# Kernel optimization log

Measured on AMD Instinct MI355X. Metric: run time of the kernel, lower is better.

## Reference

```python
import jax, jax.numpy as jnp
import numpy as np

B, T, C, H = 2, 2048, 1024, 16
D = C // H  # head_dim = 64


def setup_inputs() -> dict:
    key = jax.random.key(0)
    ks = jax.random.split(key, 5)
    s = 1.0 / np.sqrt(C)
    return {
        "x": jax.random.normal(ks[0], (B, T, C), jnp.float32),
        "Wq": jax.random.normal(ks[1], (C, C), jnp.float32) * s,
        "bq": jnp.zeros((C,), jnp.float32),
        "Wk": jax.random.normal(ks[2], (C, C), jnp.float32) * s,
        "bk": jnp.zeros((C,), jnp.float32),
        "Wv": jax.random.normal(ks[3], (C, C), jnp.float32) * s,
        "bv": jnp.zeros((C,), jnp.float32),
        "Wo": jax.random.normal(ks[4], (C, C), jnp.float32) * s,
        "bo": jnp.zeros((C,), jnp.float32),
    }


def reference(x, Wq, bq, Wk, bk, Wv, bv, Wo, bo):
    Bx, Tx, Cx = x.shape
    # torch Linear: y = x @ W.T + b
    q = (x @ Wq.T + bq).reshape(Bx, Tx, H, D).transpose(0, 2, 1, 3)  # [B,H,T,D]
    k = (x @ Wk.T + bk).reshape(Bx, Tx, H, D).transpose(0, 2, 1, 3)
    v = (x @ Wv.T + bv).reshape(Bx, Tx, H, D).transpose(0, 2, 1, 3)
    att = jnp.einsum("bhqd,bhkd->bhqk", q, k) / np.sqrt(D).astype(np.float32)
    mask = jnp.tril(jnp.ones((Tx, Tx), bool))  # causal mask [T,T]
    att = jnp.where(mask, att, -jnp.inf)
    att = jax.nn.softmax(att, axis=-1)
    out = jnp.einsum("bhqk,bhkd->bhqd", att, v)
    out = out.transpose(0, 2, 1, 3).reshape(Bx, Tx, Cx)
    return out @ Wo.T + bo
```

## Files before the change

### kernel.cpp

```cpp
#include <hip/hip_runtime.h>
#include <hip/hip_bf16.h>

#define B_ 2
#define T_ 2048
#define C_ 1024
#define H_ 16
#define D_ 64

typedef unsigned short u16;
typedef __bf16 bf16x8 __attribute__((ext_vector_type(8)));
typedef float floatx4 __attribute__((ext_vector_type(4)));

__device__ __forceinline__ float bf2f(u16 u) {
  union { unsigned int i; float f; } x; x.i = ((unsigned int)u) << 16; return x.f;
}
__device__ __forceinline__ u16 f2bf(float f) {
  union { float f; unsigned int i; } x; x.f = f;
  unsigned int r = x.i + 0x7fffu + ((x.i >> 16) & 1u);
  return (u16)(r >> 16);
}

__device__ __forceinline__ unsigned cvtpk(float lo, float hi) {
  unsigned r;
  asm("v_cvt_pk_bf16_f32 %0, %1, %2" : "=v"(r) : "v"(lo), "v"(hi));
  return r;
}

__device__ __forceinline__ void gld16(void* lds, const void* g) {
  __builtin_amdgcn_global_load_lds(
      (const __attribute__((address_space(1))) unsigned int*)g,
      (__attribute__((address_space(3))) unsigned int*)lds, 16, 0, 0);
}

#define NXF4 1048576
#define NWF4 262144

__global__ __launch_bounds__(256) void cvt_all(
    const float* __restrict__ x,  const float* __restrict__ Wq,
    const float* __restrict__ Wk, const float* __restrict__ Wv,
    const float* __restrict__ Wo, u16* __restrict__ dst_base)
{
  const int i = blockIdx.x * 256 + threadIdx.x;
  const float* src; size_t off;
  if (i < NXF4)               { src = x;  off = i; }
  else if (i < NXF4 + NWF4)   { src = Wq; off = i - NXF4; }
  else if (i < NXF4 + 2*NWF4) { src = Wk; off = i - (NXF4 + NWF4); }
  else if (i < NXF4 + 3*NWF4) { src = Wv; off = i - (NXF4 + 2*NWF4); }
  else                        { src = Wo; off = i - (NXF4 + 3*NWF4); }
  float4 f = ((const float4*)src)[off];
  ushort4 o;
  o.x = f2bf(f.x); o.y = f2bf(f.y); o.z = f2bf(f.z); o.w = f2bf(f.w);
  ((ushort4*)dst_base)[i] = o;
}

#define QSCALE 0.1803368801111f

#define MFMA16(MH, NH, BREG)                                                  \
  do {                                                                        \
    __builtin_amdgcn_s_setprio(1);                                            \
    _Pragma("unroll")                                                         \
    for (int f = 0; f < 4; ++f) {                                             \
      _Pragma("unroll")                                                       \
      for (int g = 0; g < 2; ++g) {                                           \
        acc[(MH)*4 + f][(NH)*2 + g] = __builtin_amdgcn_mfma_f32_16x16x32_bf16(\
            a[f][0], BREG[g][0], acc[(MH)*4 + f][(NH)*2 + g], 0, 0, 0);       \
        acc[(MH)*4 + f][(NH)*2 + g] = __builtin_amdgcn_mfma_f32_16x16x32_bf16(\
            a[f][1], BREG[g][1], acc[(MH)*4 + f][(NH)*2 + g], 0, 0, 0);       \
      }                                                                       \
    }                                                                         \
    __builtin_amdgcn_s_setprio(0);                                            \
  } while (0)

#define PBAR()                                                \
  do {                                                        \
    asm volatile("" ::: "memory");                            \
    __builtin_amdgcn_s_barrier();                             \
    asm volatile("s_waitcnt lgkmcnt(0)" ::: "memory");        \
  } while (0)

#define EBAR()                                                \
  do {                                                        \
    asm volatile("" ::: "memory");                            \
    __builtin_amdgcn_s_barrier();                             \
    asm volatile("" ::: "memory");                            \
  } while (0)

__global__ __launch_bounds__(512, 2) void gemm_qkv8(
    const u16* __restrict__ X, const u16* __restrict__ Wb,
    const float* __restrict__ b0, const float* __restrict__ b1,
    const float* __restrict__ b2,
    u16* __restrict__ Yq, u16* __restrict__ Yk, u16* __restrict__ Yv)
{
  __shared__ __align__(16) u16 L[65536];

  const int tid  = threadIdx.x;
  const int lane = tid & 63;
  const int m16  = lane & 15;
  const int q4   = lane >> 4;
  const int wv   = tid >> 6;
  const int wm   = wv >> 2;
  const int wn   = wv & 3;

  const int bid = blockIdx.x;
  const int xcd = bid & 7;
  const int idx = bid >> 3;
  const int bx  = (xcd & 3) * 4 + (idx & 3);
  const int by  = (xcd >> 2) * 6 + (idx >> 2);

  const u16* Abase  = X  + (size_t)bx * 256 * C_;
  const u16* Bbase  = Wb + (size_t)by * 256 * C_;
  const u16* A1base = Abase + (size_t)128 * C_;
  const u16* B1base = Bbase + (size_t)128 * C_;

  const int s0 = tid,       r0 = s0 >> 3;
  const int s1 = tid + 512, r1 = s1 >> 3;
  const int k0a = ((s0 & 7) ^ (r0 & 7)) * 8;
  const int k1a = ((s1 & 7) ^ (r1 & 7)) * 8;

#define STAGE(dsthalf, srcrows, kofs)                                         \
  do {                                                                        \
    gld16(&(dsthalf)[s0 * 8], (srcrows) + (size_t)r0 * C_ + (kofs) + k0a);    \
    gld16(&(dsthalf)[s1 * 8], (srcrows) + (size_t)r1 * C_ + (kofs) + k1a);    \
  } while (0)

  u16* buf0 = L;
  u16* buf1 = L + 32768;

  STAGE(buf0 + 16384, Bbase, 0);
  STAGE(buf0,         Abase, 0);
  STAGE(buf0 + 24576, B1base, 0);
  STAGE(buf0 + 8192,  A1base, 0);
  STAGE(buf1 + 16384, Bbase, 64);
  STAGE(buf1,         Abase, 64);
  asm volatile("s_waitcnt vmcnt(4)" ::: "memory");
  __builtin_amdgcn_s_barrier();
  asm volatile("" ::: "memory");

  floatx4 acc[8][4] = {};

  const int a0off = m16 * 64 + ((q4      ^ (lane & 7)) * 8);
  const int a1off = m16 * 64 + (((q4 + 4) ^ (lane & 7)) * 8);
  const int bro   = (wn & 1) * 4096;

  for (int i = 0; i < 16; ++i) {
    u16* buf  = (i & 1) ? buf1 : buf0;
    u16* bufn = (i & 1) ? buf0 : buf1;
    const u16* Ah = buf + wm * 8192;
    const u16* Bh = buf + 16384 + (wn >> 1) * 8192;
    const bool p1 = (i + 1) < 16;
    const bool p2 = (i + 2) < 16;
    const int  k1 = (i + 1) * 64;
    const int  k2 = (i + 2) * 64;

    bf16x8 a[4][2], bA[2][2], bB[2][2];

#pragma unroll
    for (int f = 0; f < 4; ++f) {
      a[f][0] = *(const bf16x8*)&Ah[f * 1024 + a0off];
      a[f][1] = *(const bf16x8*)&Ah[f * 1024 + a1off];
    }
#pragma unroll
    for (int g = 0; g < 2; ++g) {
      bA[g][0] = *(const bf16x8*)&Bh[bro + g * 1024 + a0off];
      bA[g][1] = *(const bf16x8*)&Bh[bro + g * 1024 + a1off];
    }
    if (p1) STAGE(bufn + 24576, B1base, k1);
    PBAR();
    MFMA16(0, 0, bA);
    EBAR();

#pragma unroll
    for (int g = 0; g < 2; ++g) {
      bB[g][0] = *(const bf16x8*)&Bh[bro + 2048 + g * 1024 + a0off];
      bB[g][1] = *(const bf16x8*)&Bh[bro + 2048 + g * 1024 + a1off];
    }
    if (p1) STAGE(bufn + 8192, A1base, k1);
    PBAR();
    MFMA16(0, 1, bB);
    EBAR();

#pragma unroll
    for (int f = 0; f < 4; ++f) {
      a[f][0] = *(const bf16x8*)&Ah[4096 + f * 1024 + a0off];
      a[f][1] = *(const bf16x8*)&Ah[4096 + f * 1024 + a1off];
    }
    if (p2) STAGE(buf + 16384, Bbase, k2);
    PBAR();
    MFMA16(1, 1, bB);
    EBAR();

    if (p2) STAGE(buf, Abase, k2);
    PBAR();
    MFMA16(1, 0, bA);
    asm volatile("" ::: "memory");
    if (p2) asm volatile("s_waitcnt vmcnt(4)" ::: "memory");
    else    asm volatile("s_waitcnt vmcnt(0)" ::: "memory");
    __builtin_amdgcn_s_barrier();
    asm volatile("" ::: "memory");
  }

  const int z    = by >> 2;
  const int nloc = (by & 3) * 256 + wn * 64;
  const float* bias = (z == 0) ? b0 : (z == 1) ? b1 : b2;
  const int mbase = bx * 256 + wm * 128 + q4 * 4;

  if (z == 2) {
#pragma unroll
    for (int nf = 0; nf < 4; ++nf) {
      const int nz = nloc + nf * 16 + m16;
      const float bv = bias[nz];
      const int h = nz >> 6, d = nz & (D_ - 1);
#pragma unroll
      for (int mf = 0; mf < 8; ++mf) {
        const int m  = mbase + mf * 16;
        const int bb = m >> 11, t = m & (T_ - 1);
        ushort4 pk;
        pk.x = f2bf(acc[mf][nf][0] + bv);
        pk.y = f2bf(acc[mf][nf][1] + bv);
        pk.z = f2bf(acc[mf][nf][2] + bv);
        pk.w = f2bf(acc[mf][nf][3] + bv);
        *(ushort4*)&Yv[(((size_t)bb * H_ + h) * D_ + d) * T_ + t] = pk;
      }
    }
  } else {
    u16* Y = z ? Yk : Yq;
    const float sc = z ? 1.0f : QSCALE;
#pragma unroll
    for (int nf = 0; nf < 4; ++nf) {
      const int nz = nloc + nf * 16 + m16;
      const float bv = bias[nz];
      const int h = nz >> 6, d = nz & (D_ - 1);
#pragma unroll
      for (int mf = 0; mf < 8; ++mf) {
        const int m  = mbase + mf * 16;
        const int bb = m >> 11, tq = m & (T_ - 1);
#pragma unroll
        for (int r = 0; r < 4; ++r) {
          Y[(((size_t)bb * H_ + h) * T_ + (tq + r)) * D_ + d] =
              f2bf((acc[mf][nf][r] + bv) * sc);
        }
      }
    }
  }
}

__global__ __launch_bounds__(256) void gemm_out(
    const u16* __restrict__ X, const u16* __restrict__ W,
    const float* __restrict__ bias, float* __restrict__ Yf)
{
  const int K = C_, N = C_;
  __shared__ __align__(16) u16 As[128 * 32];
  __shared__ __align__(16) u16 Bs[64 * 32];

  const int tid  = threadIdx.x;
  const int wv   = tid >> 6;
  const int lane = tid & 63;
  const int mcol = lane & 15;
  const int quad = lane >> 4;
  const int wr = wv >> 1, wc = wv & 1;
  const int m0 = blockIdx.x * 128;
  const int n0 = blockIdx.y * 64;

  const int srow = tid >> 2;
  const int scol = (tid & 3) * 8;
  const u16* xp0 = X + (size_t)(m0 + srow) * K + scol;
  const u16* xp1 = xp0 + (size_t)64 * K;
  const u16* wp  = W + (size_t)(n0 + srow) * K + scol;

  floatx4 acc[4][2] = {};

  for (int k0 = 0; k0 < K; k0 += 32) {
    gld16(&As[tid * 8],        xp0 + k0);
    gld16(&As[2048 + tid * 8], xp1 + k0);
    gld16(&Bs[tid * 8],        wp + k0);
    __syncthreads();

    bf16x8 a[4], b[2];
#pragma unroll
    for (int rf = 0; rf < 4; ++rf)
      a[rf] = *(const bf16x8*)&As[(wr * 64 + rf * 16 + mcol) * 32 + quad * 8];
#pragma unroll
    for (int cf = 0; cf < 2; ++cf)
      b[cf] = *(const bf16x8*)&Bs[(wc * 32 + cf * 16 + mcol) * 32 + quad * 8];
#pragma unroll
    for (int rf = 0; rf < 4; ++rf)
#pragma unroll
      for (int cf = 0; cf < 2; ++cf)
        acc[rf][cf] = __builtin_amdgcn_mfma_f32_16x16x32_bf16(
            a[rf], b[cf], acc[rf][cf], 0, 0, 0);
    __syncthreads();
  }

#pragma unroll
  for (int cf = 0; cf < 2; ++cf) {
    const int n = n0 + wc * 32 + cf * 16 + mcol;
    const float bv = bias[n];
#pragma unroll
    for (int rf = 0; rf < 4; ++rf) {
#pragma unroll
      for (int r = 0; r < 4; ++r) {
        const int m = m0 + wr * 64 + rf * 16 + quad * 4 + r;
        Yf[(size_t)m * N + n] = acc[rf][cf][r] + bv;
      }
    }
  }
}

#define KSB 4096
#define VTB 5120

__global__ __launch_bounds__(256, 4) void attn_flash(
    const u16* __restrict__ Q, const u16* __restrict__ K,
    const u16* __restrict__ Vg, u16* __restrict__ O)
{
  __shared__ __align__(16) u16 Ks[2 * KSB];
  __shared__ __align__(16) u16 Vt[2 * VTB];

  const int tid  = threadIdx.x;
  const int wv   = tid >> 6;
  const int lane = tid & 63;
  const int mcol = lane & 15;
  const int quad = lane >> 4;

  const int bx = blockIdx.x;
  const int bh = bx & 31;
  const int g  = bx >> 5;
  const int ga = g & 7, gb = g >> 3;
  const int iq = (gb == 0) ? 31 - ga : (gb == 1) ? 16 + ga
               : (gb == 2) ? 15 - ga : ga;
  const size_t base  = (size_t)bh * T_ * D_;
  const size_t vbase = (size_t)bh * D_ * T_;
  const int b = bh >> 4, h = bh & (H_ - 1);

  for (int idx = tid; idx < 16 * 64; idx += 256) {
    const u16 val = (idx < 64) ? (u16)0x3F80 : (u16)0;
    Vt[64 * 64 + idx]       = val;
    Vt[VTB + 64 * 64 + idx] = val;
  }

  const int srow = lane >> 3;
  const int sg   = (lane & 7) ^ srow;
  const int c0 = wv * 2, c1 = wv * 2 + 1;
  const int sl0 = (quad ^ (mcol & 7)) * 8;

  const size_t koff0 = base + (size_t)(c0 * 8 + srow) * D_ + sg * 8;
  const size_t koff1 = base + (size_t)(c1 * 8 + srow) * D_ + sg * 8;
  const size_t voff0 = vbase + (size_t)(c0 * 8 + srow) * T_ + sg * 8;
  const size_t voff1 = vbase + (size_t)(c1 * 8 + srow) * T_ + sg * 8;

  const u16* qg = Q + base + (size_t)(iq * 64 + wv * 16 + mcol) * D_ + quad * 8;
  const bf16x8 qf0 = *(const bf16x8*)qg;
  const bf16x8 qf1 = *(const bf16x8*)(qg + 32);

  floatx4 oacc[5] = {};

  __syncthreads();
  gld16(&Ks[c0 * 512 + lane * 8], K  + koff0);
  gld16(&Ks[c1 * 512 + lane * 8], K  + koff1);
  gld16(&Vt[c0 * 512 + lane * 8], Vg + voff0);
  gld16(&Vt[c1 * 512 + lane * 8], Vg + voff1);

  for (int j = 0; j <= iq; ++j) {
    const int cur = j & 1;
    __syncthreads();

    if (j < iq) {
      const int nb = cur ^ 1;
      const size_t kj = (size_t)(j + 1) * 64 * D_;
      const int    vj = (j + 1) * 64;
      gld16(&Ks[nb * KSB + c0 * 512 + lane * 8], K  + koff0 + kj);
      gld16(&Ks[nb * KSB + c1 * 512 + lane * 8], K  + koff1 + kj);
      gld16(&Vt[nb * VTB + c0 * 512 + lane * 8], Vg + voff0 + vj);
      gld16(&Vt[nb * VTB + c1 * 512 + lane * 8], Vg + voff1 + vj);
    }

    const u16* ksb = &Ks[cur * KSB];
    const u16* vtb = &Vt[cur * VTB];

    floatx4 sacc[4] = {};
#pragma unroll
    for (int nt = 0; nt < 4; ++nt) {
      const u16* kr = &ksb[(nt * 16 + mcol) * 64];
      bf16x8 kb0 = *(const bf16x8*)&kr[sl0];
      bf16x8 kb1 = *(const bf16x8*)&kr[sl0 ^ 32];
      sacc[nt] = __builtin_amdgcn_mfma_f32_16x16x32_bf16(kb0, qf0, sacc[nt], 0, 0, 0);
      sacc[nt] = __builtin_amdgcn_mfma_f32_16x16x32_bf16(kb1, qf1, sacc[nt], 0, 0, 0);
    }

    if (j == iq) {
      const int ql = wv * 16 + mcol;
#pragma unroll
      for (int nt = 0; nt < 4; ++nt) {
#pragma unroll
        for (int r = 0; r < 4; ++r)
          if (nt * 16 + quad * 4 + r > ql) sacc[nt][r] = -1e30f;
      }
    }

    unsigned w0[2], w1[2], w2[2], w3[2];
#pragma unroll
    for (int i = 0; i < 2; ++i) {
      w0[i] = cvtpk(exp2f(sacc[0][2*i]), exp2f(sacc[0][2*i+1]));
      w1[i] = cvtpk(exp2f(sacc[1][2*i]), exp2f(sacc[1][2*i+1]));
      w2[i] = cvtpk(exp2f(sacc[2][2*i]), exp2f(sacc[2][2*i+1]));
      w3[i] = cvtpk(exp2f(sacc[3][2*i]), exp2f(sacc[3][2*i+1]));
    }

    union { unsigned u[4]; bf16x8 v; } pa0u, pa1u;
#pragma unroll
    for (int i = 0; i < 2; ++i) {
      unsigned x = w0[i], y = w1[i];
      asm("v_permlane32_swap_b32 %0, %1" : "+v"(x), "+v"(y));
      asm("v_permlane16_swap_b32 %0, %1" : "+v"(x), "+v"(y));
      pa0u.u[i] = x; pa0u.u[i + 2] = y;
      unsigned x2 = w2[i], y2 = w3[i];
      asm("v_permlane32_swap_b32 %0, %1" : "+v"(x2), "+v"(y2));
      asm("v_permlane16_swap_b32 %0, %1" : "+v"(x2), "+v"(y2));
      pa1u.u[i] = x2; pa1u.u[i + 2] = y2;
    }
    const bf16x8 pa0 = pa0u.v;
    const bf16x8 pa1 = pa1u.v;

#pragma unroll
    for (int dt = 0; dt < 5; ++dt) {
      const u16* vr = &vtb[(dt * 16 + mcol) * 64];
      bf16x8 vb0 = *(const bf16x8*)&vr[sl0];
      bf16x8 vb1 = *(const bf16x8*)&vr[sl0 ^ 32];
      oacc[dt] = __builtin_amdgcn_mfma_f32_16x16x32_bf16(pa0, vb0, oacc[dt], 0, 0, 0);
      oacc[dt] = __builtin_amdgcn_mfma_f32_16x16x32_bf16(pa1, vb1, oacc[dt], 0, 0, 0);
    }
  }

  float invl[4];
#pragma unroll
  for (int r = 0; r < 4; ++r)
    invl[r] = 1.f / __shfl(oacc[4][r], lane & 48);
#pragma unroll
  for (int dt = 0; dt < 4; ++dt) {
    const int c = h * D_ + dt * 16 + mcol;
#pragma unroll
    for (int r = 0; r < 4; ++r) {
      const int t = iq * 64 + wv * 16 + quad * 4 + r;
      O[((size_t)b * T_ + t) * C_ + c] = f2bf(oacc[dt][r] * invl[r]);
    }
  }
}

extern "C" void kernel_launch(void* const* d_in, const int* in_sizes, int n_in,
                              void* d_out, int out_size, void* d_ws, size_t ws_size,
                              hipStream_t stream) {
  const float* x  = (const float*)d_in[0];
  const float* Wq = (const float*)d_in[1];
  const float* bq = (const float*)d_in[2];
  const float* Wk = (const float*)d_in[3];
  const float* bk = (const float*)d_in[4];
  const float* Wv = (const float*)d_in[5];
  const float* bv = (const float*)d_in[6];
  const float* Wo = (const float*)d_in[7];
  const float* bo = (const float*)d_in[8];
  float* out = (float*)d_out;

  const size_t NX = (size_t)B_ * T_ * C_;
  const size_t NW = (size_t)C_ * C_;

  u16* xb  = (u16*)d_ws;
  u16* wqb = xb  + NX;
  u16* wkb = wqb + NW;
  u16* wvb = wkb + NW;
  u16* wob = wvb + NW;
  u16* q   = wob + NW;
  u16* k   = q   + NX;
  u16* v   = k   + NX;
  u16* ctx = v   + NX;

  cvt_all<<<dim3((NXF4 + 4 * NWF4) / 256), 256, 0, stream>>>(x, Wq, Wk, Wv, Wo, xb);

  gemm_qkv8<<<dim3(192), 512, 0, stream>>>(xb, wqb, bq, bk, bv, q, k, v);

  attn_flash<<<dim3(1024), 256, 0, stream>>>(q, k, v, ctx);

  gemm_out<<<dim3(32, 16), 256, 0, stream>>>(ctx, wob, bo, out);
}
```

Before: 183.4 us.

## Double attention query tile per block to reuse K/V tiles across two row groups

Each attention block now handles 128 query rows instead of 64: each wave holds two 16-row Q fragments and runs twice the MFMAs per K/V tile loaded to LDS, so K/V global and LDS traffic per query is halved. The grid shrinks to 512 blocks, the launch-bounds occupancy hint drops to 2 blocks per CU, and the block-to-query-tile ordering is simplified. MFMA sections are wrapped in s_setprio to favour matrix issue. The risks are fewer blocks, which may leave CUs underused or load-imbalanced, and higher register pressure from doubled accumulators.

```diff
diff --git a/kernel.cpp b/kernel.cpp
--- a/kernel.cpp
+++ b/kernel.cpp
@@ -309,7 +309,7 @@
 #define KSB 4096
 #define VTB 5120
 
-__global__ __launch_bounds__(256, 4) void attn_flash(
+__global__ __launch_bounds__(256, 2) void attn_flash(
     const u16* __restrict__ Q, const u16* __restrict__ K,
     const u16* __restrict__ Vg, u16* __restrict__ O)
 {
@@ -325,9 +325,7 @@
   const int bx = blockIdx.x;
   const int bh = bx & 31;
   const int g  = bx >> 5;
-  const int ga = g & 7, gb = g >> 3;
-  const int iq = (gb == 0) ? 31 - ga : (gb == 1) ? 16 + ga
-               : (gb == 2) ? 15 - ga : ga;
+  const int iq = (g < 8) ? 15 - g : g - 8;
   const size_t base  = (size_t)bh * T_ * D_;
   const size_t vbase = (size_t)bh * D_ * T_;
   const int b = bh >> 4, h = bh & (H_ - 1);
@@ -348,11 +346,15 @@
   const size_t voff0 = vbase + (size_t)(c0 * 8 + srow) * T_ + sg * 8;
   const size_t voff1 = vbase + (size_t)(c1 * 8 + srow) * T_ + sg * 8;
 
-  const u16* qg = Q + base + (size_t)(iq * 64 + wv * 16 + mcol) * D_ + quad * 8;
-  const bf16x8 qf0 = *(const bf16x8*)qg;
-  const bf16x8 qf1 = *(const bf16x8*)(qg + 32);
-
-  floatx4 oacc[5] = {};
+  const u16* qg = Q + base + (size_t)(iq * 128 + wv * 32 + mcol) * D_ + quad * 8;
+  const bf16x8 qf[2][2] = {
+    { *(const bf16x8*)qg,               *(const bf16x8*)(qg + 32) },
+    { *(const bf16x8*)(qg + 16 * D_),   *(const bf16x8*)(qg + 16 * D_ + 32) }
+  };
+
+  floatx4 oacc[2][5] = {};
+
+  const int nj = 2 * iq + 1;
 
   __syncthreads();
   gld16(&Ks[c0 * 512 + lane * 8], K  + koff0);
@@ -360,11 +362,11 @@
   gld16(&Vt[c0 * 512 + lane * 8], Vg + voff0);
   gld16(&Vt[c1 * 512 + lane * 8], Vg + voff1);
 
-  for (int j = 0; j <= iq; ++j) {
+  for (int j = 0; j <= nj; ++j) {
     const int cur = j & 1;
     __syncthreads();
 
-    if (j < iq) {
+    if (j < nj) {
       const int nb = cur ^ 1;
       const size_t kj = (size_t)(j + 1) * 64 * D_;
       const int    vj = (j + 1) * 64;
@@ -377,71 +379,85 @@
     const u16* ksb = &Ks[cur * KSB];
     const u16* vtb = &Vt[cur * VTB];
 
-    floatx4 sacc[4] = {};
+    floatx4 sacc[2][4] = {};
+    __builtin_amdgcn_s_setprio(1);
 #pragma unroll
     for (int nt = 0; nt < 4; ++nt) {
       const u16* kr = &ksb[(nt * 16 + mcol) * 64];
       bf16x8 kb0 = *(const bf16x8*)&kr[sl0];
       bf16x8 kb1 = *(const bf16x8*)&kr[sl0 ^ 32];
-      sacc[nt] = __builtin_amdgcn_mfma_f32_16x16x32_bf16(kb0, qf0, sacc[nt], 0, 0, 0);
-      sacc[nt] = __builtin_amdgcn_mfma_f32_16x16x32_bf16(kb1, qf1, sacc[nt], 0, 0, 0);
-    }
-
-    if (j == iq) {
-      const int ql = wv * 16 + mcol;
-#pragma unroll
-      for (int nt = 0; nt < 4; ++nt) {
-#pragma unroll
-        for (int r = 0; r < 4; ++r)
-          if (nt * 16 + quad * 4 + r > ql) sacc[nt][r] = -1e30f;
-      }
-    }
-
-    unsigned w0[2], w1[2], w2[2], w3[2];
-#pragma unroll
-    for (int i = 0; i < 2; ++i) {
-      w0[i] = cvtpk(exp2f(sacc[0][2*i]), exp2f(sacc[0][2*i+1]));
-      w1[i] = cvtpk(exp2f(sacc[1][2*i]), exp2f(sacc[1][2*i+1]));
-      w2[i] = cvtpk(exp2f(sacc[2][2*i]), exp2f(sacc[2][2*i+1]));
-      w3[i] = cvtpk(exp2f(sacc[3][2*i]), exp2f(sacc[3][2*i+1]));
-    }
-
-    union { unsigned u[4]; bf16x8 v; } pa0u, pa1u;
-#pragma unroll
-    for (int i = 0; i < 2; ++i) {
-      unsigned x = w0[i], y = w1[i];
-      asm("v_permlane32_swap_b32 %0, %1" : "+v"(x), "+v"(y));
-      asm("v_permlane16_swap_b32 %0, %1" : "+v"(x), "+v"(y));
-      pa0u.u[i] = x; pa0u.u[i + 2] = y;
-      unsigned x2 = w2[i], y2 = w3[i];
-      asm("v_permlane32_swap_b32 %0, %1" : "+v"(x2), "+v"(y2));
-      asm("v_permlane16_swap_b32 %0, %1" : "+v"(x2), "+v"(y2));
-      pa1u.u[i] = x2; pa1u.u[i + 2] = y2;
-    }
-    const bf16x8 pa0 = pa0u.v;
-    const bf16x8 pa1 = pa1u.v;
-
+      sacc[0][nt] = __builtin_amdgcn_mfma_f32_16x16x32_bf16(kb0, qf[0][0], sacc[0][nt], 0, 0, 0);
+      sacc[0][nt] = __builtin_amdgcn_mfma_f32_16x16x32_bf16(kb1, qf[0][1], sacc[0][nt], 0, 0, 0);
+      sacc[1][nt] = __builtin_amdgcn_mfma_f32_16x16x32_bf16(kb0, qf[1][0], sacc[1][nt], 0, 0, 0);
+      sacc[1][nt] = __builtin_amdgcn_mfma_f32_16x16x32_bf16(kb1, qf[1][1], sacc[1][nt], 0, 0, 0);
+    }
+    __builtin_amdgcn_s_setprio(0);
+
+    const int dj = j - 2 * iq;
+    if (dj >= 0) {
+#pragma unroll
+      for (int hf = 0; hf < 2; ++hf) {
+        const int klim = wv * 32 + hf * 16 + mcol - dj * 64;
+#pragma unroll
+        for (int nt = 0; nt < 4; ++nt)
+#pragma unroll
+          for (int r = 0; r < 4; ++r)
+            if (nt * 16 + quad * 4 + r > klim) sacc[hf][nt][r] = -1e30f;
+      }
+    }
+
+    bf16x8 pa[2][2];
+#pragma unroll
+    for (int hf = 0; hf < 2; ++hf) {
+      unsigned w[4][2];
+#pragma unroll
+      for (int nt = 0; nt < 4; ++nt)
+#pragma unroll
+        for (int i = 0; i < 2; ++i)
+          w[nt][i] = cvtpk(exp2f(sacc[hf][nt][2*i]), exp2f(sacc[hf][nt][2*i+1]));
+      union { unsigned u[4]; bf16x8 v; } p0, p1;
+#pragma unroll
+      for (int i = 0; i < 2; ++i) {
+        unsigned x = w[0][i], y = w[1][i];
+        asm("v_permlane32_swap_b32 %0, %1" : "+v"(x), "+v"(y));
+        asm("v_permlane16_swap_b32 %0, %1" : "+v"(x), "+v"(y));
+        p0.u[i] = x; p0.u[i + 2] = y;
+        unsigned x2 = w[2][i], y2 = w[3][i];
+        asm("v_permlane32_swap_b32 %0, %1" : "+v"(x2), "+v"(y2));
+        asm("v_permlane16_swap_b32 %0, %1" : "+v"(x2), "+v"(y2));
+        p1.u[i] = x2; p1.u[i + 2] = y2;
+      }
+      pa[hf][0] = p0.v; pa[hf][1] = p1.v;
+    }
+
+    __builtin_amdgcn_s_setprio(1);
 #pragma unroll
     for (int dt = 0; dt < 5; ++dt) {
       const u16* vr = &vtb[(dt * 16 + mcol) * 64];
       bf16x8 vb0 = *(const bf16x8*)&vr[sl0];
       bf16x8 vb1 = *(const bf16x8*)&vr[sl0 ^ 32];
-      oacc[dt] = __builtin_amdgcn_mfma_f32_16x16x32_bf16(pa0, vb0, oacc[dt], 0, 0, 0);
-      oacc[dt] = __builtin_amdgcn_mfma_f32_16x16x32_bf16(pa1, vb1, oacc[dt], 0, 0, 0);
-    }
-  }
-
-  float invl[4];
-#pragma unroll
-  for (int r = 0; r < 4; ++r)
-    invl[r] = 1.f / __shfl(oacc[4][r], lane & 48);
-#pragma unroll
-  for (int dt = 0; dt < 4; ++dt) {
-    const int c = h * D_ + dt * 16 + mcol;
-#pragma unroll
-    for (int r = 0; r < 4; ++r) {
-      const int t = iq * 64 + wv * 16 + quad * 4 + r;
-      O[((size_t)b * T_ + t) * C_ + c] = f2bf(oacc[dt][r] * invl[r]);
+      oacc[0][dt] = __builtin_amdgcn_mfma_f32_16x16x32_bf16(pa[0][0], vb0, oacc[0][dt], 0, 0, 0);
+      oacc[0][dt] = __builtin_amdgcn_mfma_f32_16x16x32_bf16(pa[0][1], vb1, oacc[0][dt], 0, 0, 0);
+      oacc[1][dt] = __builtin_amdgcn_mfma_f32_16x16x32_bf16(pa[1][0], vb0, oacc[1][dt], 0, 0, 0);
+      oacc[1][dt] = __builtin_amdgcn_mfma_f32_16x16x32_bf16(pa[1][1], vb1, oacc[1][dt], 0, 0, 0);
+    }
+    __builtin_amdgcn_s_setprio(0);
+  }
+
+#pragma unroll
+  for (int hf = 0; hf < 2; ++hf) {
+    float invl[4];
+#pragma unroll
+    for (int r = 0; r < 4; ++r)
+      invl[r] = 1.f / __shfl(oacc[hf][4][r], lane & 48);
+#pragma unroll
+    for (int dt = 0; dt < 4; ++dt) {
+      const int c = h * D_ + dt * 16 + mcol;
+#pragma unroll
+      for (int r = 0; r < 4; ++r) {
+        const int t = iq * 128 + wv * 32 + hf * 16 + quad * 4 + r;
+        O[((size_t)b * T_ + t) * C_ + c] = f2bf(oacc[hf][dt][r] * invl[r]);
+      }
     }
   }
 }
@@ -477,7 +493,7 @@
 
   gemm_qkv8<<<dim3(192), 512, 0, stream>>>(xb, wqb, bq, bk, bv, q, k, v);
 
-  attn_flash<<<dim3(1024), 256, 0, stream>>>(q, k, v, ctx);
+  attn_flash<<<dim3(512), 256, 0, stream>>>(q, k, v, ctx);
 
   gemm_out<<<dim3(32, 16), 256, 0, stream>>>(ctx, wob, bo, out);
 }
```

Result: slower. 193.0 us (+5.2%).

## Split long causal attention rows across two blocks with a merge kernel

Applied to the files above, without the earlier changes.

Query tiles 16-31 now have their KV range split into two halves, each run by its own block. Each half writes unnormalised fp32 partial outputs and row sums to workspace, and a new merge kernel adds the halves and normalises them. The grid grows from 1024 to 1536 blocks. The goal is to even out per-block work and shorten the tail caused by the longest causal tiles. In exchange it adds an extra kernel launch, fp32 partial traffic, and relies on a fixed softmax max (no running-max rescale) so that partials can simply be summed.

```diff
diff --git a/kernel.cpp b/kernel.cpp
--- a/kernel.cpp
+++ b/kernel.cpp
@@ -311,7 +311,8 @@
 
 __global__ __launch_bounds__(256, 4) void attn_flash(
     const u16* __restrict__ Q, const u16* __restrict__ K,
-    const u16* __restrict__ Vg, u16* __restrict__ O)
+    const u16* __restrict__ Vg, u16* __restrict__ O,
+    float* __restrict__ OP, float* __restrict__ LP)
 {
   __shared__ __align__(16) u16 Ks[2 * KSB];
   __shared__ __align__(16) u16 Vt[2 * VTB];
@@ -324,10 +325,13 @@
 
   const int bx = blockIdx.x;
   const int bh = bx & 31;
-  const int g  = bx >> 5;
-  const int ga = g & 7, gb = g >> 3;
-  const int iq = (gb == 0) ? 31 - ga : (gb == 1) ? 16 + ga
-               : (gb == 2) ? 15 - ga : ga;
+  const int t  = bx >> 5;
+  const int iq = (t < 16) ? 31 - t : 47 - t;
+  const bool pc = (t < 32);
+  const int j0 = (t >= 16 && t < 32) ? 16 : 0;
+  const int j1 = (t < 16) ? 15 : iq;
+  const int ti = pc ? ((bh * 16 + (iq - 16)) * 2 + (j0 ? 1 : 0)) : 0;
+
   const size_t base  = (size_t)bh * T_ * D_;
   const size_t vbase = (size_t)bh * D_ * T_;
   const int b = bh >> 4, h = bh & (H_ - 1);
@@ -355,16 +359,20 @@
   floatx4 oacc[5] = {};
 
   __syncthreads();
-  gld16(&Ks[c0 * 512 + lane * 8], K  + koff0);
-  gld16(&Ks[c1 * 512 + lane * 8], K  + koff1);
-  gld16(&Vt[c0 * 512 + lane * 8], Vg + voff0);
-  gld16(&Vt[c1 * 512 + lane * 8], Vg + voff1);
-
-  for (int j = 0; j <= iq; ++j) {
-    const int cur = j & 1;
+  {
+    const size_t kj = (size_t)j0 * 64 * D_;
+    const int    vj = j0 * 64;
+    gld16(&Ks[c0 * 512 + lane * 8], K  + koff0 + kj);
+    gld16(&Ks[c1 * 512 + lane * 8], K  + koff1 + kj);
+    gld16(&Vt[c0 * 512 + lane * 8], Vg + voff0 + vj);
+    gld16(&Vt[c1 * 512 + lane * 8], Vg + voff1 + vj);
+  }
+
+  for (int j = j0; j <= j1; ++j) {
+    const int cur = (j - j0) & 1;
     __syncthreads();
 
-    if (j < iq) {
+    if (j < j1) {
       const int nb = cur ^ 1;
       const size_t kj = (size_t)(j + 1) * 64 * D_;
       const int    vj = (j + 1) * 64;
@@ -431,19 +439,67 @@
     }
   }
 
-  float invl[4];
-#pragma unroll
-  for (int r = 0; r < 4; ++r)
-    invl[r] = 1.f / __shfl(oacc[4][r], lane & 48);
-#pragma unroll
-  for (int dt = 0; dt < 4; ++dt) {
-    const int c = h * D_ + dt * 16 + mcol;
-#pragma unroll
-    for (int r = 0; r < 4; ++r) {
-      const int t = iq * 64 + wv * 16 + quad * 4 + r;
-      O[((size_t)b * T_ + t) * C_ + c] = f2bf(oacc[dt][r] * invl[r]);
-    }
-  }
+  if (!pc) {
+    float invl[4];
+#pragma unroll
+    for (int r = 0; r < 4; ++r)
+      invl[r] = 1.f / __shfl(oacc[4][r], lane & 48);
+#pragma unroll
+    for (int dt = 0; dt < 4; ++dt) {
+      const int c = h * D_ + dt * 16 + mcol;
+#pragma unroll
+      for (int r = 0; r < 4; ++r) {
+        const int tg = iq * 64 + wv * 16 + quad * 4 + r;
+        O[((size_t)b * T_ + tg) * C_ + c] = f2bf(oacc[dt][r] * invl[r]);
+      }
+    }
+  } else {
+    float* op = OP + (size_t)ti * 4096;
+#pragma unroll
+    for (int dt = 0; dt < 4; ++dt)
+#pragma unroll
+      for (int r = 0; r < 4; ++r)
+        op[(wv * 16 + quad * 4 + r) * 64 + dt * 16 + mcol] = oacc[dt][r];
+    if (mcol == 0) {
+#pragma unroll
+      for (int r = 0; r < 4; ++r)
+        LP[ti * 64 + wv * 16 + quad * 4 + r] = oacc[4][r];
+    }
+  }
+}
+
+__global__ __launch_bounds__(256) void attn_merge(
+    const float* __restrict__ OP, const float* __restrict__ LP,
+    u16* __restrict__ O)
+{
+  const int mb = blockIdx.x;
+  const int bh = mb & 31, qt = mb >> 5;
+  const int iq = 16 + qt;
+  const int ti0 = (bh * 16 + qt) * 2;
+  const int b = bh >> 4, h = bh & (H_ - 1);
+  const int row = threadIdx.x >> 2;
+  const int dc  = (threadIdx.x & 3) * 16;
+
+  const float l = LP[ti0 * 64 + row] + LP[(ti0 + 1) * 64 + row];
+  const float inv = 1.f / l;
+  const float* pa = OP + (size_t)ti0 * 4096 + row * 64 + dc;
+  const float* pb = pa + 4096;
+
+  const int tg = iq * 64 + row;
+  u16* o = O + ((size_t)b * T_ + tg) * C_ + h * D_ + dc;
+
+  u16 tmp[16];
+#pragma unroll
+  for (int i = 0; i < 4; ++i) {
+    const float4 a4 = ((const float4*)pa)[i];
+    const float4 b4 = ((const float4*)pb)[i];
+    tmp[i*4 + 0] = f2bf((a4.x + b4.x) * inv);
+    tmp[i*4 + 1] = f2bf((a4.y + b4.y) * inv);
+    tmp[i*4 + 2] = f2bf((a4.z + b4.z) * inv);
+    tmp[i*4 + 3] = f2bf((a4.w + b4.w) * inv);
+  }
+  *(uint4*)&o[0] = *(const uint4*)&tmp[0];
+  *(uint4*)&o[8] = *(const uint4*)&tmp[8];
 }
 
 extern "C" void kernel_launch(void* const* d_in, const int* in_sizes, int n_in,
@@ -472,12 +528,16 @@
   u16* k   = q   + NX;
   u16* v   = k   + NX;
   u16* ctx = v   + NX;
+  float* opart = (float*)(ctx + NX);
+  float* lpart = opart + (size_t)1024 * 4096;
 
   cvt_all<<<dim3((NXF4 + 4 * NWF4) / 256), 256, 0, stream>>>(x, Wq, Wk, Wv, Wo, xb);
 
   gemm_qkv8<<<dim3(192), 512, 0, stream>>>(xb, wqb, bq, bk, bv, q, k, v);
 
-  attn_flash<<<dim3(1024), 256, 0, stream>>>(q, k, v, ctx);
+  attn_flash<<<dim3(1536), 256, 0, stream>>>(q, k, v, ctx, opart, lpart);
+
+  attn_merge<<<dim3(512), 256, 0, stream>>>(opart, lpart, ctx);
 
   gemm_out<<<dim3(32, 16), 256, 0, stream>>>(ctx, wob, bo, out);
 }
```

Measured after the change: 183.9 us. About the same (+0.3%).
